# Performance work log

Hardware: AMD Instinct MI355X
Metric: run time of the kernel (lower is better)

Reference implementation:

```python
import jax, jax.numpy as jnp
import numpy as np
from jax import lax

V, H, L, F = 50304, 512, 6, 2048
SKIP_INTERVAL = 1
B, S = 4, 1024


def layer_norm(x, w, b, eps=1e-5):
    mu = jnp.mean(x, axis=-1, keepdims=True)
    var = jnp.mean(jnp.square(x - mu), axis=-1, keepdims=True)
    return (x - mu) * lax.rsqrt(var + eps) * w + b


def setup_inputs() -> dict:
    key = jax.random.key(0)
    ks = jax.random.split(key, 8)
    s = 0.02
    return {
        "input_ids": jax.random.randint(ks[0], (B, S), 0, V, dtype=jnp.int64),
        "embed_in": jax.random.normal(ks[1], (V, H), jnp.float32) * s,
        "hp_w": jax.random.normal(ks[2], (H, H), jnp.float32) * s,
        "hp_b": jnp.zeros((H,), jnp.float32),
        "ln_w": jnp.ones((L, H), jnp.float32),
        "ln_b": jnp.zeros((L, H), jnp.float32),
        "W1": jax.random.normal(ks[3], (L, H, F), jnp.float32) * s,
        "b1": jnp.zeros((L, F), jnp.float32),
        "W2": jax.random.normal(ks[4], (L, F, H), jnp.float32) * s,
        "b2": jnp.zeros((L, H), jnp.float32),
        "ln_f_w": jnp.ones((H,), jnp.float32),
        "ln_f_b": jnp.zeros((H,), jnp.float32),
        "embed_out_w": jax.random.normal(ks[5], (V, H), jnp.float32) * s,
    }


def _stack(h, ln_w, ln_b, W1, b1, W2, b2):
    # scan over L layers; each is pre-LN residual MLP: h + gelu(LN(h) @ W1 + b1) @ W2 + b2
    def step(h, p):
        lw, lb, w1, bb1, w2, bb2 = p
        y = layer_norm(h, lw, lb)
        h = h + jnp.dot(jax.nn.gelu(jnp.dot(y, w1) + bb1), w2) + bb2
        return h, None
    h, _ = lax.scan(step, h, (ln_w, ln_b, W1, b1, W2, b2))
    return h


def reference(input_ids, embed_in, hp_w, hp_b, ln_w, ln_b, W1, b1, W2, b2, ln_f_w, ln_f_b, embed_out_w):
    # forward_selective with attention_mask=None and stateless layers is
    # position-independent, so the token loop vectorizes exactly to [B,S,H].
    h = embed_in[input_ids]  # [B,S,H] gather
    h = _stack(h, ln_w, ln_b, W1, b1, W2, b2)
    for _ in range(SKIP_INTERVAL):
        h = jnp.dot(h, hp_w.T) + hp_b  # hidden_proj
        h = _stack(h, ln_w, ln_b, W1, b1, W2, b2)
    normed = layer_norm(h, ln_f_w, ln_f_b)
    logits = jnp.dot(normed, embed_out_w.T)  # [B,S,V]
    final_hidden = h[:, -1, :]  # [B,H]
    return logits, final_hidden
```

## Files before the change

### kernel.cpp

```cpp
#include <hip/hip_runtime.h>
#include <hip/hip_bf16.h>
#include <cstdint>

using bf16 = __hip_bfloat16;
typedef __bf16 bf16x8 __attribute__((ext_vector_type(8)));
typedef float f32x4 __attribute__((ext_vector_type(4)));

constexpr int Hd = 512;
constexpr int Ld = 6;
constexpr int Fd = 2048;
constexpr int Vd = 50304;
constexpr int Vpad = 50432;
constexpr int Md = 4096;

__device__ __forceinline__ unsigned short f2b(float x) {
  return __builtin_bit_cast(unsigned short, __float2bfloat16(x));
}

__device__ __forceinline__ float gelu_tanh(float x) {
  const float c = 0.7978845608028654f;
  float x3 = x * x * x;
  return 0.5f * x * (1.0f + tanhf(c * (x + 0.044715f * x3)));
}

__device__ __forceinline__ void load16_lds(const bf16* g, bf16* l) {
  __builtin_amdgcn_global_load_lds(
      (const __attribute__((address_space(1))) void*)g,
      (__attribute__((address_space(3))) void*)l, 16, 0, 0);
}

__global__ __launch_bounds__(256) void cast_weights(
    const float* __restrict__ hp, bf16* __restrict__ hpB, int n8hp,
    const float* __restrict__ eow, bf16* __restrict__ eowB, int n8cast, int n8tot) {
  int i = blockIdx.x * 256 + threadIdx.x;
  if (i < n8hp) {
    const float4* p = (const float4*)hp;
    float4 a = p[2 * i], b = p[2 * i + 1];
    uint4 o = {(unsigned)f2b(a.x) | ((unsigned)f2b(a.y) << 16),
               (unsigned)f2b(a.z) | ((unsigned)f2b(a.w) << 16),
               (unsigned)f2b(b.x) | ((unsigned)f2b(b.y) << 16),
               (unsigned)f2b(b.z) | ((unsigned)f2b(b.w) << 16)};
    ((uint4*)hpB)[i] = o;
    return;
  }
  int j = i - n8hp;
  if (j >= n8tot) return;
  if (j < n8cast) {
    const float4* p = (const float4*)eow;
    float4 a = p[2 * j], b = p[2 * j + 1];
    uint4 o = {(unsigned)f2b(a.x) | ((unsigned)f2b(a.y) << 16),
               (unsigned)f2b(a.z) | ((unsigned)f2b(a.w) << 16),
               (unsigned)f2b(b.x) | ((unsigned)f2b(b.y) << 16),
               (unsigned)f2b(b.z) | ((unsigned)f2b(b.w) << 16)};
    ((uint4*)eowB)[j] = o;
  } else {
    ((uint4*)eowB)[j] = uint4{0, 0, 0, 0};
  }
}

__global__ void transpose_cast2(const float* __restrict__ W1, bf16* __restrict__ W1t,
                                const float* __restrict__ W2, bf16* __restrict__ W2t) {
  __shared__ float tile[32][33];
  const int z = blockIdx.z;
  const bool isW1 = z < Ld;
  const int layer = isW1 ? z : z - Ld;
  const int R = isW1 ? Hd : Fd;
  const int C = isW1 ? Fd : Hd;
  const float* in = (isW1 ? W1 : W2) + (size_t)layer * R * C;
  bf16* out = (isW1 ? W1t : W2t) + (size_t)layer * R * C;
  const int tilesX = C >> 5;
  const int bx = blockIdx.x % tilesX;
  const int by = blockIdx.x / tilesX;
  int c0 = bx * 32, r0 = by * 32;
#pragma unroll
  for (int i = 0; i < 4; i++) {
    int r = r0 + threadIdx.y + i * 8;
    tile[threadIdx.y + i * 8][threadIdx.x] = in[(size_t)r * C + c0 + threadIdx.x];
  }
  __syncthreads();
#pragma unroll
  for (int i = 0; i < 4; i++) {
    int c = c0 + threadIdx.y + i * 8;
    out[(size_t)c * R + r0 + threadIdx.x] = (bf16)tile[threadIdx.x][threadIdx.y + i * 8];
  }
}

template <int MODE>
__global__ __launch_bounds__(256) void ln_rows(
    const float* __restrict__ h, const float* __restrict__ p0,
    const float* __restrict__ p1, const float* __restrict__ fb,
    const float* __restrict__ w, const float* __restrict__ b,
    float* __restrict__ hout, bf16* __restrict__ y,
    const int* __restrict__ ids, const float* __restrict__ emb,
    float* __restrict__ out2) {
  int row = blockIdx.x * 4 + (threadIdx.x >> 6);
  int lane = threadIdx.x & 63;
  size_t base = (size_t)row * Hd + lane * 8;
  float xv[8];
  if constexpr (MODE == 0) {
    *(float4*)&xv[0] = *(const float4*)(h + base);
    *(float4*)&xv[4] = *(const float4*)(h + base + 4);
  } else if constexpr (MODE == 3) {
    int id = ids[row];
    const float* src = emb + (size_t)id * Hd + lane * 8;
    *(float4*)&xv[0] = *(const float4*)(src);
    *(float4*)&xv[4] = *(const float4*)(src + 4);
    *(float4*)(hout + base) = make_float4(xv[0], xv[1], xv[2], xv[3]);
    *(float4*)(hout + base + 4) = make_float4(xv[4], xv[5], xv[6], xv[7]);
  } else {
    float4 q0 = *(const float4*)(p0 + base), q1 = *(const float4*)(p0 + base + 4);
    float4 r0 = *(const float4*)(p1 + base), r1 = *(const float4*)(p1 + base + 4);
    float4 f0 = *(const float4*)(fb + lane * 8), f1 = *(const float4*)(fb + lane * 8 + 4);
    xv[0] = q0.x + r0.x + f0.x; xv[1] = q0.y + r0.y + f0.y;
    xv[2] = q0.z + r0.z + f0.z; xv[3] = q0.w + r0.w + f0.w;
    xv[4] = q1.x + r1.x + f1.x; xv[5] = q1.y + r1.y + f1.y;
    xv[6] = q1.z + r1.z + f1.z; xv[7] = q1.w + r1.w + f1.w;
    if constexpr (MODE == 1 || MODE == 4) {
      float4 a0 = *(const float4*)(h + base), a1 = *(const float4*)(h + base + 4);
      xv[0] += a0.x; xv[1] += a0.y; xv[2] += a0.z; xv[3] += a0.w;
      xv[4] += a1.x; xv[5] += a1.y; xv[6] += a1.z; xv[7] += a1.w;
    }
    *(float4*)(hout + base) = make_float4(xv[0], xv[1], xv[2], xv[3]);
    *(float4*)(hout + base + 4) = make_float4(xv[4], xv[5], xv[6], xv[7]);
    if constexpr (MODE == 4) {
      if ((row & 1023) == 1023) {
        int bb = row >> 10;
        float* dst = out2 + (size_t)bb * Hd + lane * 8;
        *(float4*)(dst) = make_float4(xv[0], xv[1], xv[2], xv[3]);
        *(float4*)(dst + 4) = make_float4(xv[4], xv[5], xv[6], xv[7]);
      }
    }
  }
  float s = 0.f;
#pragma unroll
  for (int j = 0; j < 8; j++) s += xv[j];
#pragma unroll
  for (int off = 1; off < 64; off <<= 1) s += __shfl_xor(s, off);
  float mu = s * (1.0f / 512.0f);
  float s2 = 0.f;
#pragma unroll
  for (int j = 0; j < 8; j++) {
    xv[j] -= mu;
    s2 += xv[j] * xv[j];
  }
#pragma unroll
  for (int off = 1; off < 64; off <<= 1) s2 += __shfl_xor(s2, off);
  float scale = rsqrtf(s2 * (1.0f / 512.0f) + 1e-5f);
  float o[8];
#pragma unroll
  for (int j = 0; j < 8; j++) {
    float wj = w[lane * 8 + j], bj = b[lane * 8 + j];
    o[j] = xv[j] * scale * wj + bj;
  }
  uint4 pk = {(unsigned)f2b(o[0]) | ((unsigned)f2b(o[1]) << 16),
              (unsigned)f2b(o[2]) | ((unsigned)f2b(o[3]) << 16),
              (unsigned)f2b(o[4]) | ((unsigned)f2b(o[5]) << 16),
              (unsigned)f2b(o[6]) | ((unsigned)f2b(o[7]) << 16)};
  *(uint4*)(y + base) = pk;
}

__global__ __launch_bounds__(256) void finish2(
    const float* __restrict__ p0, const float* __restrict__ p1,
    const float* __restrict__ fb, float* __restrict__ h, bf16* __restrict__ hbf) {
  int i = blockIdx.x * 256 + threadIdx.x;
  size_t base = (size_t)i * 8;
  int col = (int)(base & 511);
  float x[8];
#pragma unroll
  for (int j = 0; j < 8; j += 4) {
    float4 a = *(const float4*)(h + base + j);
    float4 q = *(const float4*)(p0 + base + j);
    float4 r = *(const float4*)(p1 + base + j);
    float4 f = *(const float4*)(fb + col + j);
    x[j] = a.x + q.x + r.x + f.x; x[j + 1] = a.y + q.y + r.y + f.y;
    x[j + 2] = a.z + q.z + r.z + f.z; x[j + 3] = a.w + q.w + r.w + f.w;
    *(float4*)(h + base + j) = make_float4(x[j], x[j + 1], x[j + 2], x[j + 3]);
  }
  uint4 pk = {(unsigned)f2b(x[0]) | ((unsigned)f2b(x[1]) << 16),
              (unsigned)f2b(x[2]) | ((unsigned)f2b(x[3]) << 16),
              (unsigned)f2b(x[4]) | ((unsigned)f2b(x[5]) << 16),
              (unsigned)f2b(x[6]) | ((unsigned)f2b(x[7]) << 16)};
  *(uint4*)(hbf + base) = pk;
}


template <int EPI>
__global__ __launch_bounds__(256) void gemm_bt(
    const bf16* __restrict__ A, const bf16* __restrict__ Bt,
    const float* __restrict__ bias, float* __restrict__ outF,
    bf16* __restrict__ outB, int M, int N, int Klen, int lda, int ldb) {
  constexpr int ASZ = 128 * 64;
  constexpr int TILE = 2 * ASZ;
  __shared__ bf16 lds[3 * TILE];
  const int tid = threadIdx.x;
  const int wave = tid >> 6;
  const int lane = tid & 63;
  const int wm = (wave >> 1) * 64;
  const int wn = (wave & 1) * 64;

  const int bn = blockIdx.x;
  const int bm = blockIdx.y;
  const int rowA0 = bm * 128;
  const int rowB0 = bn * 128;
  const int k0 = blockIdx.z * Klen;

  const bf16* srcA[4];
  const bf16* srcB[4];
#pragma unroll
  for (int r = 0; r < 4; r++) {
    int c = r * 256 + tid;
    int row = c >> 3, d = c & 7;
    int cw = d ^ (row & 7);
    srcA[r] = A + (size_t)(rowA0 + row) * lda + k0 + cw * 8;
    srcB[r] = Bt + (size_t)(rowB0 + row) * ldb + k0 + cw * 8;
  }

  f32x4 acc[4][4];
#pragma unroll
  for (int i = 0; i < 4; i++)
#pragma unroll
    for (int j = 0; j < 4; j++) acc[i][j] = (f32x4){0.f, 0.f, 0.f, 0.f};

  const int fr = lane & 15;
  const int hi = lane >> 4;
  const int swz = fr & 7;

  auto STAGE = [&](int slot) {
    bf16* dst = lds + slot * TILE;
#pragma unroll
    for (int r = 0; r < 4; r++) {
      load16_lds(srcA[r], dst + (r * 4 + wave) * 512);
      srcA[r] += 64;
      load16_lds(srcB[r], dst + ASZ + (r * 4 + wave) * 512);
      srcB[r] += 64;
    }
  };

  STAGE(0);
  STAGE(1);
  const int nIter = Klen >> 6;
  int cur = 0, stg = 2;
  for (int it = 0; it < nIter; ++it) {
    if (it < nIter - 1)
      asm volatile("s_waitcnt vmcnt(8)" ::: "memory");
    else
      asm volatile("s_waitcnt vmcnt(0)" ::: "memory");
    __builtin_amdgcn_s_barrier();
    __builtin_amdgcn_sched_barrier(0);
    if (it + 2 < nIter) STAGE(stg);
    const bf16* lA = lds + cur * TILE;
    const bf16* lB = lA + ASZ;
#pragma unroll
    for (int ks = 0; ks < 2; ks++) {
      bf16x8 af[4], bfr[4];
#pragma unroll
      for (int f = 0; f < 4; f++) {
        int rowa = wm + f * 16 + fr;
        af[f] = *(const bf16x8*)(lA + rowa * 64 + ((ks * 4 + hi) ^ swz) * 8);
        int rowb = wn + f * 16 + fr;
        bfr[f] = *(const bf16x8*)(lB + rowb * 64 + ((ks * 4 + hi) ^ swz) * 8);
      }
#pragma unroll
      for (int i = 0; i < 4; i++)
#pragma unroll
        for (int j = 0; j < 4; j++)
          acc[i][j] = __builtin_amdgcn_mfma_f32_16x16x32_bf16(af[i], bfr[j], acc[i][j], 0, 0, 0);
    }
    cur = (cur == 2) ? 0 : cur + 1;
    stg = (stg == 2) ? 0 : stg + 1;
  }

  if constexpr (EPI == 4) outF += (size_t)blockIdx.z * M * N;
  const int orow = hi * 4;
  const int ocol = fr;
#pragma unroll
  for (int i = 0; i < 4; i++) {
#pragma unroll
    for (int j = 0; j < 4; j++) {
      int row0 = rowA0 + wm + i * 16 + orow;
      int col = rowB0 + wn + j * 16 + ocol;
#pragma unroll
      for (int q = 0; q < 4; q++) {
        float v = acc[i][j][q];
        size_t idx = (size_t)(row0 + q) * N + col;
        if constexpr (EPI == 0) {
          outB[idx] = (bf16)gelu_tanh(v + bias[col]);
        } else {
          outF[idx] = v;
        }
      }
    }
  }
}

template <int EPI>
__global__ __launch_bounds__(512) void gemm_bt256(
    const bf16* __restrict__ A, const bf16* __restrict__ Bt,
    const float* __restrict__ bias, float* __restrict__ outF,
    bf16* __restrict__ outB, int M, int N, int lda, int ldb) {
  constexpr int ASZ = 256 * 64;
  constexpr int BSZ = 128 * 64;
  constexpr int TILE = ASZ + BSZ;
  __shared__ bf16 lds[3 * TILE];
  const int tid = threadIdx.x;
  const int wave = tid >> 6;
  const int lane = tid & 63;
  const int wm = (wave >> 1) * 64;
  const int wn = (wave & 1) * 64;

  const int bn = blockIdx.x;
  const int bm = blockIdx.y;
  const int rowA0 = bm * 256;
  const int rowB0 = bn * 128;

  const bf16* srcA[4];
#pragma unroll
  for (int r = 0; r < 4; r++) {
    int c = r * 512 + tid;
    int row = c >> 3, d = c & 7;
    int cw = d ^ (row & 7);
    srcA[r] = A + (size_t)(rowA0 + row) * lda + cw * 8;
  }
  const bf16* srcB[2];
#pragma unroll
  for (int r = 0; r < 2; r++) {
    int c = r * 512 + tid;
    int row = c >> 3, d = c & 7;
    int cw = d ^ (row & 7);
    srcB[r] = Bt + (size_t)(rowB0 + row) * ldb + cw * 8;
  }

  f32x4 acc[4][4];
#pragma unroll
  for (int i = 0; i < 4; i++)
#pragma unroll
    for (int j = 0; j < 4; j++) acc[i][j] = (f32x4){0.f, 0.f, 0.f, 0.f};

  const int fr = lane & 15;
  const int hi = lane >> 4;
  const int swz = fr & 7;

  auto STAGE = [&](int slot) {
    bf16* dst = lds + slot * TILE;
#pragma unroll
    for (int r = 0; r < 4; r++) {
      load16_lds(srcA[r], dst + (r * 8 + wave) * 512);
      srcA[r] += 64;
    }
#pragma unroll
    for (int r = 0; r < 2; r++) {
      load16_lds(srcB[r], dst + ASZ + (r * 8 + wave) * 512);
      srcB[r] += 64;
    }
  };

  STAGE(0);
  STAGE(1);
  const int nIter = 512 >> 6;
  int cur = 0, stg = 2;
  for (int it = 0; it < nIter; ++it) {
    if (it < nIter - 1)
      asm volatile("s_waitcnt vmcnt(6)" ::: "memory");
    else
      asm volatile("s_waitcnt vmcnt(0)" ::: "memory");
    __builtin_amdgcn_s_barrier();
    __builtin_amdgcn_sched_barrier(0);
    if (it + 2 < nIter) STAGE(stg);
    const bf16* lA = lds + cur * TILE;
    const bf16* lB = lA + ASZ;
#pragma unroll
    for (int ks = 0; ks < 2; ks++) {
      bf16x8 af[4], bfr[4];
#pragma unroll
      for (int f = 0; f < 4; f++) {
        int rowa = wm + f * 16 + fr;
        af[f] = *(const bf16x8*)(lA + rowa * 64 + ((ks * 4 + hi) ^ swz) * 8);
        int rowb = wn + f * 16 + fr;
        bfr[f] = *(const bf16x8*)(lB + rowb * 64 + ((ks * 4 + hi) ^ swz) * 8);
      }
#pragma unroll
      for (int i = 0; i < 4; i++)
#pragma unroll
        for (int j = 0; j < 4; j++)
          acc[i][j] = __builtin_amdgcn_mfma_f32_16x16x32_bf16(af[i], bfr[j], acc[i][j], 0, 0, 0);
    }
    cur = (cur == 2) ? 0 : cur + 1;
    stg = (stg == 2) ? 0 : stg + 1;
  }

  const int orow = hi * 4;
  const int ocol = fr;
#pragma unroll
  for (int i = 0; i < 4; i++) {
#pragma unroll
    for (int j = 0; j < 4; j++) {
      int row0 = rowA0 + wm + i * 16 + orow;
      int col = rowB0 + wn + j * 16 + ocol;
#pragma unroll
      for (int q = 0; q < 4; q++) {
        float v = acc[i][j][q];
        size_t idx = (size_t)(row0 + q) * N + col;
        if constexpr (EPI == 0) {
          outB[idx] = (bf16)gelu_tanh(v + bias[col]);
        } else {
          outF[idx] = v;
        }
      }
    }
  }
}

__global__ __launch_bounds__(512, 1) void gemm_logits(
    const bf16* __restrict__ A, const bf16* __restrict__ Bt,
    float* __restrict__ outF, int M, int N, int lda, int ldb) {
  constexpr int ASZ = 256 * 64;
  constexpr int TILE = 2 * ASZ;
  __shared__ bf16 lds[2 * TILE];
  const int tid = threadIdx.x;
  const int wave = tid >> 6;
  const int lane = tid & 63;
  const int wm = (wave >> 2) * 128;
  const int wn = (wave & 3) * 64;

  const int per = gridDim.x >> 3;
  const int wg = (blockIdx.x & 7) * per + (blockIdx.x >> 3);
  const int bm = wg & 15;
  const int bn = wg >> 4;
  const int rowA0 = bm * 256;
  const int rowB0 = bn * 256;

  const bf16* srcA[4];
  const bf16* srcB[4];
#pragma unroll
  for (int r = 0; r < 4; r++) {
    int c = r * 512 + tid;
    int row = c >> 3, d = c & 7;
    int cw = d ^ (row & 7);
    srcA[r] = A + (size_t)(rowA0 + row) * lda + cw * 8;
    srcB[r] = Bt + (size_t)(rowB0 + row) * ldb + cw * 8;
  }

  f32x4 acc[8][4];
#pragma unroll
  for (int i = 0; i < 8; i++)
#pragma unroll
    for (int j = 0; j < 4; j++) acc[i][j] = (f32x4){0.f, 0.f, 0.f, 0.f};

  const int fr = lane & 15;
  const int hi = lane >> 4;
  const int swz = fr & 7;

  auto STAGE = [&](int slot) {
    bf16* dst = lds + slot * TILE;
#pragma unroll
    for (int r = 0; r < 4; r++) {
      load16_lds(srcA[r], dst + (r * 8 + wave) * 512);
      srcA[r] += 64;
      load16_lds(srcB[r], dst + ASZ + (r * 8 + wave) * 512);
      srcB[r] += 64;
    }
  };

  STAGE(0);
  const int nIter = 512 >> 6;
  for (int it = 0; it < nIter; ++it) {
    const int cur = it & 1;
    if (it + 1 < nIter) STAGE(cur ^ 1);
    if (it + 1 < nIter)
      asm volatile("s_waitcnt vmcnt(8)" ::: "memory");
    else
      asm volatile("s_waitcnt vmcnt(0)" ::: "memory");
    __builtin_amdgcn_s_barrier();
    __builtin_amdgcn_sched_barrier(0);
    const bf16* lA = lds + cur * TILE;
    const bf16* lB = lA + ASZ;
#pragma unroll
    for (int ks = 0; ks < 2; ks++) {
      bf16x8 af[8], bfr[4];
#pragma unroll
      for (int f = 0; f < 8; f++) {
        int rowa = wm + f * 16 + fr;
        af[f] = *(const bf16x8*)(lA + rowa * 64 + ((ks * 4 + hi) ^ swz) * 8);
      }
#pragma unroll
      for (int f = 0; f < 4; f++) {
        int rowb = wn + f * 16 + fr;
        bfr[f] = *(const bf16x8*)(lB + rowb * 64 + ((ks * 4 + hi) ^ swz) * 8);
      }
#pragma unroll
      for (int i = 0; i < 8; i++)
#pragma unroll
        for (int j = 0; j < 4; j++)
          acc[i][j] = __builtin_amdgcn_mfma_f32_16x16x32_bf16(af[i], bfr[j], acc[i][j], 0, 0, 0);
    }
    __builtin_amdgcn_s_barrier();
  }

  const int orow = hi * 4;
  const int ocol = fr;
#pragma unroll
  for (int i = 0; i < 8; i++) {
#pragma unroll
    for (int j = 0; j < 4; j++) {
      int row0 = rowA0 + wm + i * 16 + orow;
      int col = rowB0 + wn + j * 16 + ocol;
      if (col < N) {
#pragma unroll
        for (int q = 0; q < 4; q++)
          outF[(size_t)(row0 + q) * N + col] = acc[i][j][q];
      }
    }
  }
}

extern "C" void kernel_launch(void* const* d_in, const int* in_sizes, int n_in,
                              void* d_out, int out_size, void* d_ws, size_t ws_size,
                              hipStream_t stream) {
  const int* ids = (const int*)d_in[0];
  const float* emb = (const float*)d_in[1];
  const float* hp_w = (const float*)d_in[2];
  const float* hp_b = (const float*)d_in[3];
  const float* ln_w = (const float*)d_in[4];
  const float* ln_b = (const float*)d_in[5];
  const float* W1 = (const float*)d_in[6];
  const float* b1 = (const float*)d_in[7];
  const float* W2 = (const float*)d_in[8];
  const float* b2 = (const float*)d_in[9];
  const float* lnf_w = (const float*)d_in[10];
  const float* lnf_b = (const float*)d_in[11];
  const float* eow = (const float*)d_in[12];
  float* out = (float*)d_out;

  char* ws = (char*)d_ws;
  float* h = (float*)(ws);
  bf16* ybf = (bf16*)(ws + (8u << 20));
  bf16* abf = (bf16*)(ws + (12u << 20));
  bf16* W1t = (bf16*)(ws + (28u << 20));
  bf16* W2t = (bf16*)(ws + (40u << 20));
  bf16* hpwB = (bf16*)(ws + (52u << 20));
  bf16* eowB = (bf16*)(ws + (53u << 20));

  float* p0 = out;
  float* p1 = out + (size_t)Md * Hd;

  {
    int n8hp = Hd * Hd / 8;
    int n8cast = Vd * Hd / 8, n8tot = Vpad * Hd / 8;
    int n8all = n8hp + n8tot;
    cast_weights<<<dim3((n8all + 255) / 256), dim3(256), 0, stream>>>(
        hp_w, hpwB, n8hp, eow, eowB, n8cast, n8tot);
  }
  transpose_cast2<<<dim3((Fd / 32) * (Hd / 32), 1, 2 * Ld), dim3(32, 8), 0, stream>>>(
      W1, W1t, W2, W2t);

  auto layer = [&](int l, int mode, const float* fb, const float* lw, const float* lb) {
    if (mode == 1)
      ln_rows<1><<<dim3(Md / 4), dim3(256), 0, stream>>>(h, p0, p1, fb, lw, lb, h, ybf,
                                                         nullptr, nullptr, nullptr);
    else if (mode == 2)
      ln_rows<2><<<dim3(Md / 4), dim3(256), 0, stream>>>(h, p0, p1, fb, lw, lb, h, ybf,
                                                         nullptr, nullptr, nullptr);
    else
      ln_rows<3><<<dim3(Md / 4), dim3(256), 0, stream>>>(h, p0, p1, fb, lw, lb, h, ybf,
                                                         ids, emb, nullptr);
    gemm_bt256<0><<<dim3(Fd / 128, Md / 256), dim3(512), 0, stream>>>(
        ybf, W1t + (size_t)l * Fd * Hd, b1 + (size_t)l * Fd, (float*)nullptr, abf,
        Md, Fd, Hd, Hd);
    gemm_bt<4><<<dim3(Hd / 128, Md / 128, 2), dim3(256), 0, stream>>>(
        abf, W2t + (size_t)l * Hd * Fd, (const float*)nullptr, p0, (bf16*)nullptr,
        Md, Hd, Fd / 2, Fd, Fd);
  };

  layer(0, 3, nullptr, ln_w, ln_b);
  for (int l = 1; l < Ld; l++)
    layer(l, 1, b2 + (size_t)(l - 1) * Hd, ln_w + (size_t)l * Hd, ln_b + (size_t)l * Hd);
  finish2<<<dim3(Md * Hd / 8 / 256), dim3(256), 0, stream>>>(
      p0, p1, b2 + (size_t)(Ld - 1) * Hd, h, ybf);

  gemm_bt<4><<<dim3(Hd / 128, Md / 128, 2), dim3(256), 0, stream>>>(
      ybf, hpwB, (const float*)nullptr, p0, (bf16*)nullptr, Md, Hd, Hd / 2, Hd, Hd);

  layer(0, 2, hp_b, ln_w, ln_b);
  for (int l = 1; l < Ld; l++)
    layer(l, 1, b2 + (size_t)(l - 1) * Hd, ln_w + (size_t)l * Hd, ln_b + (size_t)l * Hd);

  ln_rows<4><<<dim3(Md / 4), dim3(256), 0, stream>>>(
      h, p0, p1, b2 + (size_t)(Ld - 1) * Hd, lnf_w, lnf_b, h, ybf,
      nullptr, nullptr, out + (size_t)Md * Vd);
  gemm_logits<<<dim3((Vpad / 256) * (Md / 256)), dim3(512), 0, stream>>>(
      ybf, eowB, out, Md, Vd, Hd, Hd);
}
```

Measured before the change: 930.2 us.

## Fuse second MLP GEMM with residual add and next-layer LayerNorm

Replaces the split-K W2 GEMM plus the separate ln_rows and finish2 kernels with one gemm2_ln kernel. Each block computes 64 full rows of 512 columns, adds the bias and residual, and reduces mean and variance across waves in LDS. It then writes h and the bf16 normalized input for the next layer, and the hidden_proj GEMM uses the same kernel. This removes the fp32 partial-sum round trips through p0/p1 and several launches, but it launches only 64 large blocks using about 147 KB of LDS, which leaves many CUs idle. Variance is now computed as E[x^2]-mu^2.

Result: slower. 1.325 ms (+42.4%).

```diff
diff --git a/kernel.cpp b/kernel.cpp
--- a/kernel.cpp
+++ b/kernel.cpp
@@ -85,52 +85,20 @@
   }
 }
 
-template <int MODE>
-__global__ __launch_bounds__(256) void ln_rows(
-    const float* __restrict__ h, const float* __restrict__ p0,
-    const float* __restrict__ p1, const float* __restrict__ fb,
+__global__ __launch_bounds__(256) void ln_gather(
+    const int* __restrict__ ids, const float* __restrict__ emb,
     const float* __restrict__ w, const float* __restrict__ b,
-    float* __restrict__ hout, bf16* __restrict__ y,
-    const int* __restrict__ ids, const float* __restrict__ emb,
-    float* __restrict__ out2) {
+    float* __restrict__ hout, bf16* __restrict__ y) {
   int row = blockIdx.x * 4 + (threadIdx.x >> 6);
   int lane = threadIdx.x & 63;
   size_t base = (size_t)row * Hd + lane * 8;
+  int id = ids[row];
+  const float* src = emb + (size_t)id * Hd + lane * 8;
   float xv[8];
-  if constexpr (MODE == 0) {
-    *(float4*)&xv[0] = *(const float4*)(h + base);
-    *(float4*)&xv[4] = *(const float4*)(h + base + 4);
-  } else if constexpr (MODE == 3) {
-    int id = ids[row];
-    const float* src = emb + (size_t)id * Hd + lane * 8;
-    *(float4*)&xv[0] = *(const float4*)(src);
-    *(float4*)&xv[4] = *(const float4*)(src + 4);
-    *(float4*)(hout + base) = make_float4(xv[0], xv[1], xv[2], xv[3]);
-    *(float4*)(hout + base + 4) = make_float4(xv[4], xv[5], xv[6], xv[7]);
-  } else {
-    float4 q0 = *(const float4*)(p0 + base), q1 = *(const float4*)(p0 + base + 4);
-    float4 r0 = *(const float4*)(p1 + base), r1 = *(const float4*)(p1 + base + 4);
-    float4 f0 = *(const float4*)(fb + lane * 8), f1 = *(const float4*)(fb + lane * 8 + 4);
-    xv[0] = q0.x + r0.x + f0.x; xv[1] = q0.y + r0.y + f0.y;
-    xv[2] = q0.z + r0.z + f0.z; xv[3] = q0.w + r0.w + f0.w;
-    xv[4] = q1.x + r1.x + f1.x; xv[5] = q1.y + r1.y + f1.y;
-    xv[6] = q1.z + r1.z + f1.z; xv[7] = q1.w + r1.w + f1.w;
-    if constexpr (MODE == 1 || MODE == 4) {
-      float4 a0 = *(const float4*)(h + base), a1 = *(const float4*)(h + base + 4);
-      xv[0] += a0.x; xv[1] += a0.y; xv[2] += a0.z; xv[3] += a0.w;
-      xv[4] += a1.x; xv[5] += a1.y; xv[6] += a1.z; xv[7] += a1.w;
-    }
-    *(float4*)(hout + base) = make_float4(xv[0], xv[1], xv[2], xv[3]);
-    *(float4*)(hout + base + 4) = make_float4(xv[4], xv[5], xv[6], xv[7]);
-    if constexpr (MODE == 4) {
-      if ((row & 1023) == 1023) {
-        int bb = row >> 10;
-        float* dst = out2 + (size_t)bb * Hd + lane * 8;
-        *(float4*)(dst) = make_float4(xv[0], xv[1], xv[2], xv[3]);
-        *(float4*)(dst + 4) = make_float4(xv[4], xv[5], xv[6], xv[7]);
-      }
-    }
-  }
+  *(float4*)&xv[0] = *(const float4*)(src);
+  *(float4*)&xv[4] = *(const float4*)(src + 4);
+  *(float4*)(hout + base) = make_float4(xv[0], xv[1], xv[2], xv[3]);
+  *(float4*)(hout + base + 4) = make_float4(xv[4], xv[5], xv[6], xv[7]);
   float s = 0.f;
 #pragma unroll
   for (int j = 0; j < 8; j++) s += xv[j];
@@ -148,149 +116,12 @@
   float scale = rsqrtf(s2 * (1.0f / 512.0f) + 1e-5f);
   float o[8];
 #pragma unroll
-  for (int j = 0; j < 8; j++) {
-    float wj = w[lane * 8 + j], bj = b[lane * 8 + j];
-    o[j] = xv[j] * scale * wj + bj;
-  }
+  for (int j = 0; j < 8; j++) o[j] = xv[j] * scale * w[lane * 8 + j] + b[lane * 8 + j];
   uint4 pk = {(unsigned)f2b(o[0]) | ((unsigned)f2b(o[1]) << 16),
               (unsigned)f2b(o[2]) | ((unsigned)f2b(o[3]) << 16),
               (unsigned)f2b(o[4]) | ((unsigned)f2b(o[5]) << 16),
               (unsigned)f2b(o[6]) | ((unsigned)f2b(o[7]) << 16)};
   *(uint4*)(y + base) = pk;
-}
-
-__global__ __launch_bounds__(256) void finish2(
-    const float* __restrict__ p0, const float* __restrict__ p1,
-    const float* __restrict__ fb, float* __restrict__ h, bf16* __restrict__ hbf) {
-  int i = blockIdx.x * 256 + threadIdx.x;
-  size_t base = (size_t)i * 8;
-  int col = (int)(base & 511);
-  float x[8];
-#pragma unroll
-  for (int j = 0; j < 8; j += 4) {
-    float4 a = *(const float4*)(h + base + j);
-    float4 q = *(const float4*)(p0 + base + j);
-    float4 r = *(const float4*)(p1 + base + j);
-    float4 f = *(const float4*)(fb + col + j);
-    x[j] = a.x + q.x + r.x + f.x; x[j + 1] = a.y + q.y + r.y + f.y;
-    x[j + 2] = a.z + q.z + r.z + f.z; x[j + 3] = a.w + q.w + r.w + f.w;
-    *(float4*)(h + base + j) = make_float4(x[j], x[j + 1], x[j + 2], x[j + 3]);
-  }
-  uint4 pk = {(unsigned)f2b(x[0]) | ((unsigned)f2b(x[1]) << 16),
-              (unsigned)f2b(x[2]) | ((unsigned)f2b(x[3]) << 16),
-              (unsigned)f2b(x[4]) | ((unsigned)f2b(x[5]) << 16),
-              (unsigned)f2b(x[6]) | ((unsigned)f2b(x[7]) << 16)};
-  *(uint4*)(hbf + base) = pk;
-}
-
-
-template <int EPI>
-__global__ __launch_bounds__(256) void gemm_bt(
-    const bf16* __restrict__ A, const bf16* __restrict__ Bt,
-    const float* __restrict__ bias, float* __restrict__ outF,
-    bf16* __restrict__ outB, int M, int N, int Klen, int lda, int ldb) {
-  constexpr int ASZ = 128 * 64;
-  constexpr int TILE = 2 * ASZ;
-  __shared__ bf16 lds[3 * TILE];
-  const int tid = threadIdx.x;
-  const int wave = tid >> 6;
-  const int lane = tid & 63;
-  const int wm = (wave >> 1) * 64;
-  const int wn = (wave & 1) * 64;
-
-  const int bn = blockIdx.x;
-  const int bm = blockIdx.y;
-  const int rowA0 = bm * 128;
-  const int rowB0 = bn * 128;
-  const int k0 = blockIdx.z * Klen;
-
-  const bf16* srcA[4];
-  const bf16* srcB[4];
-#pragma unroll
-  for (int r = 0; r < 4; r++) {
-    int c = r * 256 + tid;
-    int row = c >> 3, d = c & 7;
-    int cw = d ^ (row & 7);
-    srcA[r] = A + (size_t)(rowA0 + row) * lda + k0 + cw * 8;
-    srcB[r] = Bt + (size_t)(rowB0 + row) * ldb + k0 + cw * 8;
-  }
-
-  f32x4 acc[4][4];
-#pragma unroll
-  for (int i = 0; i < 4; i++)
-#pragma unroll
-    for (int j = 0; j < 4; j++) acc[i][j] = (f32x4){0.f, 0.f, 0.f, 0.f};
-
-  const int fr = lane & 15;
-  const int hi = lane >> 4;
-  const int swz = fr & 7;
-
-  auto STAGE = [&](int slot) {
-    bf16* dst = lds + slot * TILE;
-#pragma unroll
-    for (int r = 0; r < 4; r++) {
-      load16_lds(srcA[r], dst + (r * 4 + wave) * 512);
-      srcA[r] += 64;
-      load16_lds(srcB[r], dst + ASZ + (r * 4 + wave) * 512);
-      srcB[r] += 64;
-    }
-  };
-
-  STAGE(0);
-  STAGE(1);
-  const int nIter = Klen >> 6;
-  int cur = 0, stg = 2;
-  for (int it = 0; it < nIter; ++it) {
-    if (it < nIter - 1)
-      asm volatile("s_waitcnt vmcnt(8)" ::: "memory");
-    else
-      asm volatile("s_waitcnt vmcnt(0)" ::: "memory");
-    __builtin_amdgcn_s_barrier();
-    __builtin_amdgcn_sched_barrier(0);
-    if (it + 2 < nIter) STAGE(stg);
-    const bf16* lA = lds + cur * TILE;
-    const bf16* lB = lA + ASZ;
-#pragma unroll
-    for (int ks = 0; ks < 2; ks++) {
-      bf16x8 af[4], bfr[4];
-#pragma unroll
-      for (int f = 0; f < 4; f++) {
-        int rowa = wm + f * 16 + fr;
-        af[f] = *(const bf16x8*)(lA + rowa * 64 + ((ks * 4 + hi) ^ swz) * 8);
-        int rowb = wn + f * 16 + fr;
-        bfr[f] = *(const bf16x8*)(lB + rowb * 64 + ((ks * 4 + hi) ^ swz) * 8);
-      }
-#pragma unroll
-      for (int i = 0; i < 4; i++)
-#pragma unroll
-        for (int j = 0; j < 4; j++)
-          acc[i][j] = __builtin_amdgcn_mfma_f32_16x16x32_bf16(af[i], bfr[j], acc[i][j], 0, 0, 0);
-    }
-    cur = (cur == 2) ? 0 : cur + 1;
-    stg = (stg == 2) ? 0 : stg + 1;
-  }
-
-  if constexpr (EPI == 4) outF += (size_t)blockIdx.z * M * N;
-  const int orow = hi * 4;
-  const int ocol = fr;
-#pragma unroll
-  for (int i = 0; i < 4; i++) {
-#pragma unroll
-    for (int j = 0; j < 4; j++) {
-      int row0 = rowA0 + wm + i * 16 + orow;
-      int col = rowB0 + wn + j * 16 + ocol;
-#pragma unroll
-      for (int q = 0; q < 4; q++) {
-        float v = acc[i][j][q];
-        size_t idx = (size_t)(row0 + q) * N + col;
-        if constexpr (EPI == 0) {
-          outB[idx] = (bf16)gelu_tanh(v + bias[col]);
-        } else {
-          outF[idx] = v;
-        }
-      }
-    }
-  }
 }
 
 template <int EPI>
@@ -405,6 +236,180 @@
         } else {
           outF[idx] = v;
         }
+      }
+    }
+  }
+}
+
+template <int MODE>
+__global__ __launch_bounds__(256) void gemm2_ln(
+    const bf16* __restrict__ A, const bf16* __restrict__ Bt,
+    const float* __restrict__ fb, const float* __restrict__ lw,
+    const float* __restrict__ lb, float* __restrict__ h,
+    bf16* __restrict__ y, float* __restrict__ out2, int K) {
+  constexpr int ASZ = 64 * 64;
+  constexpr int BSZ = 512 * 64;
+  constexpr int TILE = ASZ + BSZ;
+  __shared__ bf16 lds[2 * TILE];
+  const int tid = threadIdx.x;
+  const int wave = tid >> 6;
+  const int lane = tid & 63;
+  const int fr = lane & 15;
+  const int hi = lane >> 4;
+  const int swz = fr & 7;
+  const int rowA0 = blockIdx.x * 64;
+  const int wn = wave * 128;
+
+  const int rsel = tid >> 3;
+  const int cw = (tid & 7) ^ (rsel & 7);
+  const bf16* srcA0 = A + (size_t)(rowA0 + rsel) * K + cw * 8;
+  const bf16* srcB0 = Bt + (size_t)rsel * K + cw * 8;
+  int koff = 0;
+
+  f32x4 acc[4][8];
+#pragma unroll
+  for (int i = 0; i < 4; i++)
+#pragma unroll
+    for (int j = 0; j < 8; j++) acc[i][j] = (f32x4){0.f, 0.f, 0.f, 0.f};
+
+  auto STAGE = [&]() {
+    int slot = (koff >> 6) & 1;
+    bf16* dst = lds + slot * TILE;
+#pragma unroll
+    for (int r = 0; r < 2; r++)
+      load16_lds(srcA0 + (size_t)(r * 32) * K + koff, dst + (r * 256 + tid) * 8);
+#pragma unroll
+    for (int r = 0; r < 16; r++)
+      load16_lds(srcB0 + (size_t)(r * 32) * K + koff, dst + ASZ + (r * 256 + tid) * 8);
+    koff += 64;
+  };
+
+  STAGE();
+  const int nIter = K >> 6;
+  for (int it = 0; it < nIter; ++it) {
+    const int cur = it & 1;
+    if (it + 1 < nIter) {
+      STAGE();
+      asm volatile("s_waitcnt vmcnt(18)" ::: "memory");
+    } else {
+      asm volatile("s_waitcnt vmcnt(0)" ::: "memory");
+    }
+    __builtin_amdgcn_s_barrier();
+    __builtin_amdgcn_sched_barrier(0);
+    const bf16* lA = lds + cur * TILE;
+    const bf16* lB = lA + ASZ;
+#pragma unroll
+    for (int ks = 0; ks < 2; ks++) {
+      bf16x8 af[4], bfr[8];
+#pragma unroll
+      for (int i = 0; i < 4; i++) {
+        int rowa = i * 16 + fr;
+        af[i] = *(const bf16x8*)(lA + rowa * 64 + ((ks * 4 + hi) ^ swz) * 8);
+      }
+#pragma unroll
+      for (int j = 0; j < 8; j++) {
+        int rowb = wn + j * 16 + fr;
+        bfr[j] = *(const bf16x8*)(lB + rowb * 64 + ((ks * 4 + hi) ^ swz) * 8);
+      }
+#pragma unroll
+      for (int i = 0; i < 4; i++)
+#pragma unroll
+        for (int j = 0; j < 8; j++)
+          acc[i][j] = __builtin_amdgcn_mfma_f32_16x16x32_bf16(af[i], bfr[j], acc[i][j], 0, 0, 0);
+    }
+    __builtin_amdgcn_s_barrier();
+  }
+
+  float fbv[8], lwv[8], lbv[8];
+#pragma unroll
+  for (int j = 0; j < 8; j++) {
+    int col = wn + j * 16 + fr;
+    fbv[j] = fb[col];
+    if constexpr (MODE != 1) {
+      lwv[j] = lw[col];
+      lbv[j] = lb[col];
+    }
+  }
+
+  float sum[4][4], sq[4][4];
+#pragma unroll
+  for (int i = 0; i < 4; i++) {
+#pragma unroll
+    for (int q = 0; q < 4; q++) {
+      sum[i][q] = 0.f;
+      sq[i][q] = 0.f;
+      int row = rowA0 + i * 16 + hi * 4 + q;
+#pragma unroll
+      for (int j = 0; j < 8; j++) {
+        float v = acc[i][j][q] + fbv[j];
+        if constexpr (MODE != 2) v += h[(size_t)row * Hd + wn + j * 16 + fr];
+        acc[i][j][q] = v;
+        sum[i][q] += v;
+        sq[i][q] += v * v;
+      }
+    }
+  }
+
+  if constexpr (MODE != 1) {
+#pragma unroll
+    for (int i = 0; i < 4; i++)
+#pragma unroll
+      for (int q = 0; q < 4; q++) {
+        float s = sum[i][q], s2 = sq[i][q];
+#pragma unroll
+        for (int off = 1; off < 16; off <<= 1) {
+          s += __shfl_xor(s, off);
+          s2 += __shfl_xor(s2, off);
+        }
+        sum[i][q] = s;
+        sq[i][q] = s2;
+      }
+    float* red = (float*)lds;
+    if (fr == 0) {
+#pragma unroll
+      for (int i = 0; i < 4; i++)
+#pragma unroll
+        for (int q = 0; q < 4; q++) {
+          int rl = i * 16 + hi * 4 + q;
+          red[(wave * 64 + rl) * 2 + 0] = sum[i][q];
+          red[(wave * 64 + rl) * 2 + 1] = sq[i][q];
+        }
+    }
+    __syncthreads();
+#pragma unroll
+    for (int i = 0; i < 4; i++)
+#pragma unroll
+      for (int q = 0; q < 4; q++) {
+        int rl = i * 16 + hi * 4 + q;
+        float S = 0.f, S2 = 0.f;
+#pragma unroll
+        for (int w = 0; w < 4; w++) {
+          S += red[(w * 64 + rl) * 2 + 0];
+          S2 += red[(w * 64 + rl) * 2 + 1];
+        }
+        float mu = S * (1.0f / 512.0f);
+        float var = S2 * (1.0f / 512.0f) - mu * mu;
+        sum[i][q] = mu;
+        sq[i][q] = rsqrtf(var + 1e-5f);
+      }
+  }
+
+#pragma unroll
+  for (int i = 0; i < 4; i++) {
+#pragma unroll
+    for (int q = 0; q < 4; q++) {
+      int row = rowA0 + i * 16 + hi * 4 + q;
+      bool tail = (MODE == 3) && ((row & 1023) == 1023);
+#pragma unroll
+      for (int j = 0; j < 8; j++) {
+        int col = wn + j * 16 + fr;
+        float v = acc[i][j][q];
+        if constexpr (MODE != 3) h[(size_t)row * Hd + col] = v;
+        float o;
+        if constexpr (MODE == 1) o = v;
+        else o = (v - sum[i][q]) * sq[i][q] * lwv[j] + lbv[j];
+        y[(size_t)row * Hd + col] = (bf16)o;
+        if (tail) out2[(size_t)(row >> 10) * Hd + col] = v;
       }
     }
   }
@@ -540,9 +545,6 @@
   bf16* hpwB = (bf16*)(ws + (52u << 20));
   bf16* eowB = (bf16*)(ws + (53u << 20));
 
-  float* p0 = out;
-  float* p1 = out + (size_t)Md * Hd;
-
   {
     int n8hp = Hd * Hd / 8;
     int n8cast = Vd * Hd / 8, n8tot = Vpad * Hd / 8;
@@ -553,40 +555,43 @@
   transpose_cast2<<<dim3((Fd / 32) * (Hd / 32), 1, 2 * Ld), dim3(32, 8), 0, stream>>>(
       W1, W1t, W2, W2t);
 
-  auto layer = [&](int l, int mode, const float* fb, const float* lw, const float* lb) {
-    if (mode == 1)
-      ln_rows<1><<<dim3(Md / 4), dim3(256), 0, stream>>>(h, p0, p1, fb, lw, lb, h, ybf,
-                                                         nullptr, nullptr, nullptr);
-    else if (mode == 2)
-      ln_rows<2><<<dim3(Md / 4), dim3(256), 0, stream>>>(h, p0, p1, fb, lw, lb, h, ybf,
-                                                         nullptr, nullptr, nullptr);
-    else
-      ln_rows<3><<<dim3(Md / 4), dim3(256), 0, stream>>>(h, p0, p1, fb, lw, lb, h, ybf,
-                                                         ids, emb, nullptr);
+  ln_gather<<<dim3(Md / 4), dim3(256), 0, stream>>>(ids, emb, ln_w, ln_b, h, ybf);
+
+  auto gemm1 = [&](int l) {
     gemm_bt256<0><<<dim3(Fd / 128, Md / 256), dim3(512), 0, stream>>>(
         ybf, W1t + (size_t)l * Fd * Hd, b1 + (size_t)l * Fd, (float*)nullptr, abf,
         Md, Fd, Hd, Hd);
-    gemm_bt<4><<<dim3(Hd / 128, Md / 128, 2), dim3(256), 0, stream>>>(
-        abf, W2t + (size_t)l * Hd * Fd, (const float*)nullptr, p0, (bf16*)nullptr,
-        Md, Hd, Fd / 2, Fd, Fd);
   };
 
-  layer(0, 3, nullptr, ln_w, ln_b);
-  for (int l = 1; l < Ld; l++)
-    layer(l, 1, b2 + (size_t)(l - 1) * Hd, ln_w + (size_t)l * Hd, ln_b + (size_t)l * Hd);
-  finish2<<<dim3(Md * Hd / 8 / 256), dim3(256), 0, stream>>>(
-      p0, p1, b2 + (size_t)(Ld - 1) * Hd, h, ybf);
-
-  gemm_bt<4><<<dim3(Hd / 128, Md / 128, 2), dim3(256), 0, stream>>>(
-      ybf, hpwB, (const float*)nullptr, p0, (bf16*)nullptr, Md, Hd, Hd / 2, Hd, Hd);
-
-  layer(0, 2, hp_b, ln_w, ln_b);
-  for (int l = 1; l < Ld; l++)
-    layer(l, 1, b2 + (size_t)(l - 1) * Hd, ln_w + (size_t)l * Hd, ln_b + (size_t)l * Hd);
-
-  ln_rows<4><<<dim3(Md / 4), dim3(256), 0, stream>>>(
-      h, p0, p1, b2 + (size_t)(Ld - 1) * Hd, lnf_w, lnf_b, h, ybf,
-      nullptr, nullptr, out + (size_t)Md * Vd);
+  for (int l = 0; l < Ld; l++) {
+    gemm1(l);
+    if (l < Ld - 1)
+      gemm2_ln<0><<<dim3(Md / 64), dim3(256), 0, stream>>>(
+          abf, W2t + (size_t)l * Hd * Fd, b2 + (size_t)l * Hd,
+          ln_w + (size_t)(l + 1) * Hd, ln_b + (size_t)(l + 1) * Hd, h, ybf,
+          (float*)nullptr, Fd);
+    else
+      gemm2_ln<1><<<dim3(Md / 64), dim3(256), 0, stream>>>(
+          abf, W2t + (size_t)l * Hd * Fd, b2 + (size_t)l * Hd,
+          (const float*)nullptr, (const float*)nullptr, h, ybf, (float*)nullptr, Fd);
+  }
+
+  gemm2_ln<2><<<dim3(Md / 64), dim3(256), 0, stream>>>(
+      ybf, hpwB, hp_b, ln_w, ln_b, h, ybf, (float*)nullptr, Hd);
+
+  for (int l = 0; l < Ld; l++) {
+    gemm1(l);
+    if (l < Ld - 1)
+      gemm2_ln<0><<<dim3(Md / 64), dim3(256), 0, stream>>>(
+          abf, W2t + (size_t)l * Hd * Fd, b2 + (size_t)l * Hd,
+          ln_w + (size_t)(l + 1) * Hd, ln_b + (size_t)(l + 1) * Hd, h, ybf,
+          (float*)nullptr, Fd);
+    else
+      gemm2_ln<3><<<dim3(Md / 64), dim3(256), 0, stream>>>(
+          abf, W2t + (size_t)l * Hd * Fd, b2 + (size_t)l * Hd, lnf_w, lnf_b, h, ybf,
+          out + (size_t)Md * Vd, Fd);
+  }
+
   gemm_logits<<<dim3((Vpad / 256) * (Md / 256)), dim3(512), 0, stream>>>(
       ybf, eowB, out, Md, Vd, Hd, Hd);
 }
```
